# Performance work log

Measured on AMD Instinct MI355X. Metric: run time of the kernel, lower is better.

## Reference

```python
import jax, jax.numpy as jnp
import numpy as np

N_NODES = 32768
N_EDGES = 65536
NODE_IN = 4
EDGE_IN = 4
HIDDEN = 64
LN_EPS = 1e-5


def setup_inputs() -> dict:
    key = jax.random.key(0)
    ks = jax.random.split(key, 20)
    s = 0.05
    inp = {
        "x": jax.random.normal(ks[0], (N_NODES, NODE_IN), dtype=jnp.float32),
        "edge_attr": jax.random.normal(ks[1], (N_EDGES, EDGE_IN), dtype=jnp.float32),
        "edge_index": jax.random.randint(ks[2], (2, N_EDGES), 0, N_NODES, dtype=jnp.int64),
        "batch": jnp.zeros((N_NODES,), dtype=jnp.int64),
        # layer 1: edge MLP edge_in->64->node_in*hidden, root [node_in,hidden]
        "e1_w1": jax.random.normal(ks[3], (EDGE_IN, 64), dtype=jnp.float32) * s,
        "e1_b1": jnp.zeros((64,), jnp.float32),
        "e1_w2": jax.random.normal(ks[4], (64, NODE_IN * HIDDEN), dtype=jnp.float32) * s,
        "e1_b2": jnp.zeros((NODE_IN * HIDDEN,), jnp.float32),
        "root1": jax.random.normal(ks[5], (NODE_IN, HIDDEN), dtype=jnp.float32) * s,
        "bias1": jnp.zeros((HIDDEN,), jnp.float32),
        "ln1_g": jnp.ones((HIDDEN,), jnp.float32),
        "ln1_b": jnp.zeros((HIDDEN,), jnp.float32),
        # layer 2: edge MLP edge_in->128->hidden*hidden, root [hidden,hidden]
        "e2_w1": jax.random.normal(ks[6], (EDGE_IN, 128), dtype=jnp.float32) * s,
        "e2_b1": jnp.zeros((128,), jnp.float32),
        "e2_w2": jax.random.normal(ks[7], (128, HIDDEN * HIDDEN), dtype=jnp.float32) * s,
        "e2_b2": jnp.zeros((HIDDEN * HIDDEN,), jnp.float32),
        "root2": jax.random.normal(ks[8], (HIDDEN, HIDDEN), dtype=jnp.float32) * s,
        "bias2": jnp.zeros((HIDDEN,), jnp.float32),
        "ln2_g": jnp.ones((HIDDEN,), jnp.float32),
        "ln2_b": jnp.zeros((HIDDEN,), jnp.float32),
    }
    return inp


def _nnconv(x, src, dst, edge_attr, ew1, eb1, ew2, eb2, root, bias, n_nodes):
    # edge-conditioned weights: [E, in_ch, out_ch]
    in_ch = x.shape[1]
    out_ch = root.shape[1]
    h = jax.nn.relu(edge_attr @ ew1 + eb1) @ ew2 + eb2
    W = h.reshape(-1, in_ch, out_ch)
    # gather source features, per-edge matvec, scatter-mean to dest
    msg = jnp.einsum('ei,eio->eo', x[src], W)  # [E, out_ch]
    summed = jax.ops.segment_sum(msg, dst, num_segments=n_nodes)
    cnt = jax.ops.segment_sum(jnp.ones((dst.shape[0],), msg.dtype), dst,
                              num_segments=n_nodes)
    agg = summed / jnp.maximum(cnt, 1.0)[:, None]
    return agg + x @ root + bias


def _layernorm(x, g, b):
    m = x.mean(-1, keepdims=True)
    v = ((x - m) ** 2).mean(-1, keepdims=True)
    return (x - m) * jax.lax.rsqrt(v + LN_EPS) * g + b


def reference(x, edge_attr, e1_w1, e1_b1, e1_w2, e1_b2, root1, bias1, ln1_g, ln1_b,
              e2_w1, e2_b1, e2_w2, e2_b2, root2, bias2, ln2_g, ln2_b,
              edge_index, batch):
    src, dst = edge_index[0], edge_index[1]
    n = x.shape[0]
    h = _nnconv(x, src, dst, edge_attr, e1_w1, e1_b1, e1_w2, e1_b2, root1, bias1, n)
    h = _layernorm(jax.nn.relu(h), ln1_g, ln1_b)  # dropout = identity (eval)
    h = _nnconv(h, src, dst, edge_attr, e2_w1, e2_b1, e2_w2, e2_b2, root2, bias2, n)
    h = _layernorm(jax.nn.relu(h), ln2_g, ln2_b)
    # global mean pool (single graph -> [1, hidden])
    gs = jax.ops.segment_sum(h, batch, num_segments=1)
    gc = jax.ops.segment_sum(jnp.ones((n,), h.dtype), batch, num_segments=1)
    return gs / jnp.maximum(gc, 1.0)[:, None]
```

## Files before the change

### kernel.cpp

```cpp
#include <hip/hip_runtime.h>

#define N_NODES 32768
#define N_EDGES 65536

typedef float f32x4 __attribute__((ext_vector_type(4)));
typedef short s16x8 __attribute__((ext_vector_type(8)));

__device__ __forceinline__ unsigned short f2bf(float f){
  unsigned u = __float_as_uint(f);
  u += 0x7FFFu + ((u >> 16) & 1u);
  return (unsigned short)(u >> 16);
}
__device__ __forceinline__ float bf2f(unsigned short b){
  return __uint_as_float(((unsigned)b) << 16);
}

__global__ void k_zero(int* __restrict__ p, int n){
  int i = blockIdx.x * 256 + threadIdx.x;
  if (i < n) p[i] = 0;
}

__global__ void k_prep(const float* __restrict__ e2_w2, const float* __restrict__ e2_b2,
                       const float* __restrict__ e1_w2,
                       unsigned short* __restrict__ W2f, unsigned short* __restrict__ T1g){
  int idx = blockIdx.x * 256 + threadIdx.x;
  if (idx < 129 * 4096){
    int j = idx & 7, l = (idx >> 3) & 63, half = (idx >> 9) & 1, ot = (idx >> 10) & 3, kf = idx >> 12;
    int i = half * 32 + ((l >> 4) << 3) + j;
    int o = ot * 16 + (l & 15);
    float v = (kf < 128) ? e2_w2[kf * 4096 + i * 64 + o] : e2_b2[i * 64 + o];
    W2f[idx] = f2bf(v);
  } else if (idx < 129 * 4096 + 16384){
    int t = idx - 129 * 4096;
    int j = t & 7, l = (t >> 3) & 63, half = (t >> 9) & 1, ot = (t >> 10) & 3, i = t >> 12;
    int kf = half * 32 + ((l >> 4) << 3) + j;
    int o = ot * 16 + (l & 15);
    T1g[t] = f2bf(e1_w2[kf * 256 + i * 64 + o]);
  }
}

__global__ void k_hist(const int* __restrict__ ei, int* __restrict__ cnti){
  int i = blockIdx.x * 256 + threadIdx.x;
  if (i < N_EDGES) atomicAdd(cnti + ei[N_EDGES + i], 1);
}

__global__ void k_scanA(const int* __restrict__ cnti, int* __restrict__ lex, int* __restrict__ bsum){
  const int tid = threadIdx.x;
  int n = blockIdx.x * 256 + tid;
  int c = cnti[n];
  int v = c;
  int lane = tid & 63;
  #pragma unroll
  for (int d = 1; d < 64; d <<= 1){
    int t = __shfl_up(v, d);
    if (lane >= d) v += t;
  }
  __shared__ int wsum[4];
  if (lane == 63) wsum[tid >> 6] = v;
  __syncthreads();
  int off = 0;
  for (int i = 0; i < (tid >> 6); ++i) off += wsum[i];
  lex[n] = off + v - c;
  if (tid == 255) bsum[blockIdx.x] = off + v;
}

__global__ void k_scanB(const int* __restrict__ bsum, int* __restrict__ bsx){
  const int tid = threadIdx.x;
  int c = bsum[tid];
  int v = c;
  int lane = tid & 63;
  #pragma unroll
  for (int d = 1; d < 64; d <<= 1){
    int t = __shfl_up(v, d);
    if (lane >= d) v += t;
  }
  __shared__ int w0;
  if (tid == 63) w0 = v;
  __syncthreads();
  if (tid >= 64) v += w0;
  bsx[tid] = v - c;
}

__global__ void k_fill(const int* __restrict__ ei, const int* __restrict__ lex,
                       const int* __restrict__ bsx, int* __restrict__ cur,
                       int* __restrict__ eslot){
  int e = blockIdx.x * 256 + threadIdx.x;
  if (e < N_EDGES){
    int d = ei[N_EDGES + e];
    int base = lex[d] + bsx[d >> 8];
    eslot[e] = base + atomicAdd(cur + d, 1);
  }
}

__launch_bounds__(256, 4)
__global__ void k_msg1(const float* __restrict__ x, const float* __restrict__ ea,
                       const int* __restrict__ ei, const int* __restrict__ eslot,
                       const float* __restrict__ e1_w1, const float* __restrict__ e1_b1,
                       const float* __restrict__ e1_b2,
                       const unsigned short* __restrict__ T1g,
                       float* __restrict__ msg)
{
  __shared__ float eas[64 * 4];
  __shared__ unsigned short F1f[8 * 64 * 8];
  const int tid = threadIdx.x;
  const int eblk = blockIdx.x * 64;

  if (tid < 64) ((float4*)eas)[tid] = ((const float4*)ea)[eblk + tid];
  __syncthreads();
  {
    int kf = tid & 63, eh = tid >> 6;
    float w0 = e1_w1[kf], w1 = e1_w1[64 + kf], w2 = e1_w1[128 + kf], w3 = e1_w1[192 + kf];
    float bb = e1_b1[kf];
    int half = kf >> 5, hi = (kf >> 3) & 3, j = kf & 7;
    for (int e = eh * 16; e < eh * 16 + 16; ++e){
      float s = fmaf(eas[e*4+0], w0, fmaf(eas[e*4+1], w1, fmaf(eas[e*4+2], w2, fmaf(eas[e*4+3], w3, bb))));
      F1f[(((e >> 4) * 2 + half) * 64 + hi * 16 + (e & 15)) * 8 + j] = f2bf(fmaxf(s, 0.f));
    }
  }
  __syncthreads();

  const int l = tid & 63, lm = l & 15, lg = l >> 4;
  const int ot = tid >> 6;
  int esl[4];
  float xs[4][4];
  s16x8 bf[4][2];
  #pragma unroll
  for (int et = 0; et < 4; ++et){
    int e = eblk + et * 16 + lm;
    int s = ei[e];
    esl[et] = eslot[e];
    float4 xv = *(const float4*)(x + s * 4);
    xs[et][0] = xv.x; xs[et][1] = xv.y; xs[et][2] = xv.z; xs[et][3] = xv.w;
    bf[et][0] = ((const s16x8*)F1f)[(et * 2 + 0) * 64 + l];
    bf[et][1] = ((const s16x8*)F1f)[(et * 2 + 1) * 64 + l];
  }
  f32x4 acc[4];
  #pragma unroll
  for (int et = 0; et < 4; ++et) acc[et] = (f32x4){0.f, 0.f, 0.f, 0.f};

  #pragma unroll
  for (int i = 0; i < 4; ++i){
    const s16x8* p = (const s16x8*)(T1g + (i * 4 + ot) * 1024);
    s16x8 a0 = p[l], a1 = p[64 + l];
    #pragma unroll
    for (int et = 0; et < 4; ++et){
      f32x4 g = (f32x4){0.f, 0.f, 0.f, 0.f};
      g = __builtin_amdgcn_mfma_f32_16x16x32_bf16(a0, bf[et][0], g, 0, 0, 0);
      g = __builtin_amdgcn_mfma_f32_16x16x32_bf16(a1, bf[et][1], g, 0, 0, 0);
      acc[et] += xs[et][i] * g;
    }
  }
  float b2v[4][4];
  #pragma unroll
  for (int i = 0; i < 4; ++i)
    #pragma unroll
    for (int r = 0; r < 4; ++r) b2v[i][r] = e1_b2[i * 64 + ot * 16 + lg * 4 + r];
  #pragma unroll
  for (int et = 0; et < 4; ++et)
    #pragma unroll
    for (int r = 0; r < 4; ++r)
      #pragma unroll
      for (int i = 0; i < 4; ++i) acc[et][r] = fmaf(xs[et][i], b2v[i][r], acc[et][r]);

  #pragma unroll
  for (int et = 0; et < 4; ++et)
    *(f32x4*)(msg + (size_t)esl[et] * 64 + ot * 16 + lg * 4) = acc[et];
}

__launch_bounds__(256)
__global__ void k_node1(const float* __restrict__ x, const float* __restrict__ root1,
                        const float* __restrict__ bias1, const float* __restrict__ lng,
                        const float* __restrict__ lnb, const int* __restrict__ cnti,
                        const int* __restrict__ lex, const int* __restrict__ bsx,
                        const float* __restrict__ msg, unsigned short* __restrict__ h1b)
{
  const int tid = threadIdx.x;
  int n = blockIdx.x * 4 + (tid >> 6);
  int o = tid & 63;
  int rp = lex[n] + bsx[n >> 8];
  int deg = cnti[n];
  float s = 0.f;
  for (int j = 0; j < deg; ++j) s += msg[(size_t)(rp + j) * 64 + o];
  float v = s * (1.f / fmaxf((float)deg, 1.f));
  float4 xv = *(const float4*)(x + n * 4);
  v = fmaf(xv.x, root1[o], v);
  v = fmaf(xv.y, root1[64 + o], v);
  v = fmaf(xv.z, root1[128 + o], v);
  v = fmaf(xv.w, root1[192 + o], v);
  v = fmaxf(v + bias1[o], 0.f);
  float m = v;
  #pragma unroll
  for (int d = 32; d > 0; d >>= 1) m += __shfl_xor(m, d);
  m *= (1.f / 64.f);
  float dd = v - m;
  float var = dd * dd;
  #pragma unroll
  for (int d = 32; d > 0; d >>= 1) var += __shfl_xor(var, d);
  var *= (1.f / 64.f);
  float out = dd * rsqrtf(var + 1e-5f) * lng[o] + lnb[o];
  h1b[n * 64 + o] = f2bf(out);
}

__launch_bounds__(512, 4)
__global__ void k_msg2(const float* __restrict__ ea, const int* __restrict__ ei,
                       const int* __restrict__ eslot,
                       const float* __restrict__ e2_w1, const float* __restrict__ e2_b1,
                       const unsigned short* __restrict__ h1b,
                       const unsigned short* __restrict__ W2f,
                       float* __restrict__ msg)
{
  __shared__ float eas[128 * 4];
  __shared__ float F2s[128 * 132];
  const int tid = threadIdx.x;
  const int eblk = blockIdx.x * 128;
  if (tid < 128) ((float4*)eas)[tid] = ((const float4*)ea)[eblk + tid];
  __syncthreads();
  {
    int kf = tid & 127, q = tid >> 7;
    float w0 = e2_w1[kf], w1 = e2_w1[128 + kf], w2 = e2_w1[256 + kf], w3 = e2_w1[384 + kf];
    float bb = e2_b1[kf];
    for (int e = q * 32; e < q * 32 + 32; ++e){
      float s = fmaf(eas[e*4+0], w0, fmaf(eas[e*4+1], w1, fmaf(eas[e*4+2], w2, fmaf(eas[e*4+3], w3, bb))));
      F2s[e * 132 + kf] = fmaxf(s, 0.f);
    }
  }
  __syncthreads();

  const int w = tid >> 6, l = tid & 63, lm = l & 15, lg = l >> 4;
  const int ot = w >> 1, eh = w & 1;
  int f2base[4], esl[4];
  s16x8 bh[4][2];
  #pragma unroll
  for (int et = 0; et < 4; ++et){
    int eloc = eh * 64 + et * 16 + lm;
    int e = eblk + eloc;
    int s = ei[e];
    esl[et] = eslot[e];
    f2base[et] = eloc * 132;
    const s16x8* hp = (const s16x8*)(h1b + s * 64);
    bh[et][0] = hp[lg];
    bh[et][1] = hp[4 + lg];
  }
  f32x4 acc[4];
  #pragma unroll
  for (int et = 0; et < 4; ++et) acc[et] = (f32x4){0.f, 0.f, 0.f, 0.f};

  const unsigned short* wbase = W2f + ot * 1024;
  s16x8 A0[2], A1[2], A2[2], A3[2];
  #define LOADA(DST, KF) { const s16x8* p = (const s16x8*)(wbase + (size_t)(KF) * 4096); DST[0] = p[l]; DST[1] = p[64 + l]; }
  #define STEP(A, J) { \
    _Pragma("unroll") \
    for (int et = 0; et < 4; ++et){ \
      float f2v = f2c[et][J]; \
      f32x4 g = (f32x4){0.f, 0.f, 0.f, 0.f}; \
      g = __builtin_amdgcn_mfma_f32_16x16x32_bf16(A[0], bh[et][0], g, 0, 0, 0); \
      g = __builtin_amdgcn_mfma_f32_16x16x32_bf16(A[1], bh[et][1], g, 0, 0, 0); \
      acc[et] += f2v * g; \
    } }

  LOADA(A0, 0)
  LOADA(A1, 1)
  #pragma unroll 1
  for (int ch = 0; ch < 32; ++ch){
    f32x4 f2c[4];
    #pragma unroll
    for (int et = 0; et < 4; ++et) f2c[et] = *(const f32x4*)&F2s[f2base[et] + ch * 4];
    const int kf = ch * 4;
    LOADA(A2, kf + 2)
    STEP(A0, 0)
    LOADA(A3, kf + 3)
    STEP(A1, 1)
    LOADA(A0, kf + 4)
    STEP(A2, 2)
    const int k5 = (kf + 5 > 128) ? 128 : kf + 5;
    LOADA(A1, k5)
    STEP(A3, 3)
  }
  #pragma unroll
  for (int et = 0; et < 4; ++et){
    acc[et] = __builtin_amdgcn_mfma_f32_16x16x32_bf16(A0[0], bh[et][0], acc[et], 0, 0, 0);
    acc[et] = __builtin_amdgcn_mfma_f32_16x16x32_bf16(A0[1], bh[et][1], acc[et], 0, 0, 0);
  }
  #undef LOADA
  #undef STEP

  #pragma unroll
  for (int et = 0; et < 4; ++et)
    *(f32x4*)(msg + (size_t)esl[et] * 64 + ot * 16 + lg * 4) = acc[et];
}

__launch_bounds__(1024)
__global__ void k_node2(const unsigned short* __restrict__ h1b, const float* __restrict__ root2,
                        const float* __restrict__ bias2, const float* __restrict__ lng,
                        const float* __restrict__ lnb, const int* __restrict__ cnti,
                        const int* __restrict__ lex, const int* __restrict__ bsx,
                        const float* __restrict__ msg, float* __restrict__ partial)
{
  const int tid = threadIdx.x;
  int n = blockIdx.x * 16 + (tid >> 6);
  int o = tid & 63;
  int rp = lex[n] + bsx[n >> 8];
  int deg = cnti[n];
  float s = 0.f;
  for (int j = 0; j < deg; ++j) s += msg[(size_t)(rp + j) * 64 + o];
  float v = s * (1.f / fmaxf((float)deg, 1.f));
  const s16x8* hp = (const s16x8*)(h1b + n * 64);
  #pragma unroll
  for (int c = 0; c < 8; ++c){
    s16x8 hv = hp[c];
    #pragma unroll
    for (int j = 0; j < 8; ++j)
      v = fmaf(bf2f((unsigned short)hv[j]), root2[(c * 8 + j) * 64 + o], v);
  }
  v = fmaxf(v + bias2[o], 0.f);
  float m = v;
  #pragma unroll
  for (int d = 32; d > 0; d >>= 1) m += __shfl_xor(m, d);
  m *= (1.f / 64.f);
  float dd = v - m;
  float var = dd * dd;
  #pragma unroll
  for (int d = 32; d > 0; d >>= 1) var += __shfl_xor(var, d);
  var *= (1.f / 64.f);
  float out = dd * rsqrtf(var + 1e-5f) * lng[o] + lnb[o];
  __shared__ float pp[16][64];
  pp[tid >> 6][o] = out;
  __syncthreads();
  if (tid < 64){
    float t = 0.f;
    #pragma unroll
    for (int k = 0; k < 16; ++k) t += pp[k][tid];
    partial[blockIdx.x * 64 + tid] = t;
  }
}

__launch_bounds__(1024)
__global__ void k_out(const float* __restrict__ partial, float* __restrict__ out){
  const int tid = threadIdx.x;
  int o = tid & 63, q = tid >> 6;
  float s = 0.f;
  for (int b = q; b < 2048; b += 16) s += partial[b * 64 + o];
  __shared__ float pp[16][64];
  pp[q][o] = s;
  __syncthreads();
  if (tid < 64){
    float t = 0.f;
    #pragma unroll
    for (int k = 0; k < 16; ++k) t += pp[k][tid];
    out[tid] = t * (1.f / 32768.f);
  }
}

extern "C" void kernel_launch(void* const* d_in, const int* in_sizes, int n_in,
                              void* d_out, int out_size, void* d_ws, size_t ws_size,
                              hipStream_t stream)
{
  const float* x      = (const float*)d_in[0];
  const float* ea     = (const float*)d_in[1];
  const int*   ei     = (const int*)  d_in[2];
  const float* e1_w1  = (const float*)d_in[4];
  const float* e1_b1  = (const float*)d_in[5];
  const float* e1_w2  = (const float*)d_in[6];
  const float* e1_b2  = (const float*)d_in[7];
  const float* root1  = (const float*)d_in[8];
  const float* bias1  = (const float*)d_in[9];
  const float* ln1g   = (const float*)d_in[10];
  const float* ln1b   = (const float*)d_in[11];
  const float* e2_w1  = (const float*)d_in[12];
  const float* e2_b1  = (const float*)d_in[13];
  const float* e2_w2  = (const float*)d_in[14];
  const float* e2_b2  = (const float*)d_in[15];
  const float* root2  = (const float*)d_in[16];
  const float* bias2  = (const float*)d_in[17];
  const float* ln2g   = (const float*)d_in[18];
  const float* ln2b   = (const float*)d_in[19];

  char* w = (char*)d_ws;
  float*          msg     = (float*)(w);
  unsigned short* h1b     = (unsigned short*)(w + 16777216);
  unsigned short* W2f     = (unsigned short*)(w + 20971520);
  unsigned short* T1g     = (unsigned short*)(w + 22028288);
  int*            cnti    = (int*)(w + 22061056);
  int*            cur     = (int*)(w + 22192128);
  int*            lex     = (int*)(w + 22323200);
  int*            bsx     = (int*)(w + 22454272);
  int*            bsum    = (int*)(w + 22454784);
  int*            eslot   = (int*)(w + 22455296);
  float*          partial = (float*)(w + 22717440);

  k_zero <<<256, 256, 0, stream>>>(cnti, 65536);
  k_prep <<<2128, 256, 0, stream>>>(e2_w2, e2_b2, e1_w2, W2f, T1g);
  k_hist <<<256, 256, 0, stream>>>(ei, cnti);
  k_scanA<<<128, 256, 0, stream>>>(cnti, lex, bsum);
  k_scanB<<<1, 128, 0, stream>>>(bsum, bsx);
  k_fill <<<256, 256, 0, stream>>>(ei, lex, bsx, cur, eslot);
  k_msg1 <<<1024, 256, 0, stream>>>(x, ea, ei, eslot, e1_w1, e1_b1, e1_b2, T1g, msg);
  k_node1<<<8192, 256, 0, stream>>>(x, root1, bias1, ln1g, ln1b, cnti, lex, bsx, msg, h1b);
  k_msg2 <<<512, 512, 0, stream>>>(ea, ei, eslot, e2_w1, e2_b1, h1b, W2f, msg);
  k_node2<<<2048, 1024, 0, stream>>>(h1b, root2, bias2, ln2g, ln2b, cnti, lex, bsx, msg, partial);
  k_out  <<<1, 1024, 0, stream>>>(partial, (float*)d_out);
}
```

Before: 175.9 us.

## Halve k_msg2 block size so each wave covers all 128 edges with grouped weight prefetch

k_msg2 now runs 256 threads (4 waves) per block instead of 512, and each wave handles one 16-wide output tile across all 128 edges (8 edge tiles) rather than 64 edges. This doubles reuse of each loaded W2f fragment and halves global weight traffic per block. Weight loads are also grouped four k-steps at a time and double-buffered (GA/GB), and the source-feature gathers are moved ahead of the F2 computation to overlap latency. The cost is much higher register pressure (8 accumulators, 8x2 B fragments, 2x4x2 A buffers), and occupancy is lower with launch bounds of (256,2).

```diff
diff --git a/kernel.cpp b/kernel.cpp
--- a/kernel.cpp
+++ b/kernel.cpp
@@ -201,7 +201,7 @@
   h1b[n * 64 + o] = f2bf(out);
 }
 
-__launch_bounds__(512, 4)
+__launch_bounds__(256, 2)
 __global__ void k_msg2(const float* __restrict__ ea, const int* __restrict__ ei,
                        const int* __restrict__ eslot,
                        const float* __restrict__ e2_w1, const float* __restrict__ e2_b1,
@@ -213,79 +213,79 @@
   __shared__ float F2s[128 * 132];
   const int tid = threadIdx.x;
   const int eblk = blockIdx.x * 128;
+  const int l = tid & 63, lm = l & 15, lg = l >> 4;
+  const int ot = tid >> 6;
+
+  int esl[8];
+  s16x8 bh[8][2];
+  #pragma unroll
+  for (int et = 0; et < 8; ++et){
+    int e = eblk + et * 16 + lm;
+    int s = ei[e];
+    esl[et] = eslot[e];
+    const s16x8* hp = (const s16x8*)(h1b + s * 64);
+    bh[et][0] = hp[lg];
+    bh[et][1] = hp[4 + lg];
+  }
+
   if (tid < 128) ((float4*)eas)[tid] = ((const float4*)ea)[eblk + tid];
   __syncthreads();
   {
     int kf = tid & 127, q = tid >> 7;
     float w0 = e2_w1[kf], w1 = e2_w1[128 + kf], w2 = e2_w1[256 + kf], w3 = e2_w1[384 + kf];
     float bb = e2_b1[kf];
-    for (int e = q * 32; e < q * 32 + 32; ++e){
+    for (int e = q * 64; e < q * 64 + 64; ++e){
       float s = fmaf(eas[e*4+0], w0, fmaf(eas[e*4+1], w1, fmaf(eas[e*4+2], w2, fmaf(eas[e*4+3], w3, bb))));
       F2s[e * 132 + kf] = fmaxf(s, 0.f);
     }
   }
   __syncthreads();
 
-  const int w = tid >> 6, l = tid & 63, lm = l & 15, lg = l >> 4;
-  const int ot = w >> 1, eh = w & 1;
-  int f2base[4], esl[4];
-  s16x8 bh[4][2];
-  #pragma unroll
-  for (int et = 0; et < 4; ++et){
-    int eloc = eh * 64 + et * 16 + lm;
-    int e = eblk + eloc;
-    int s = ei[e];
-    esl[et] = eslot[e];
-    f2base[et] = eloc * 132;
-    const s16x8* hp = (const s16x8*)(h1b + s * 64);
-    bh[et][0] = hp[lg];
-    bh[et][1] = hp[4 + lg];
-  }
-  f32x4 acc[4];
-  #pragma unroll
-  for (int et = 0; et < 4; ++et) acc[et] = (f32x4){0.f, 0.f, 0.f, 0.f};
+  f32x4 acc[8];
+  #pragma unroll
+  for (int et = 0; et < 8; ++et) acc[et] = (f32x4){0.f, 0.f, 0.f, 0.f};
 
   const unsigned short* wbase = W2f + ot * 1024;
-  s16x8 A0[2], A1[2], A2[2], A3[2];
-  #define LOADA(DST, KF) { const s16x8* p = (const s16x8*)(wbase + (size_t)(KF) * 4096); DST[0] = p[l]; DST[1] = p[64 + l]; }
-  #define STEP(A, J) { \
+  s16x8 GA[4][2], GB[4][2];
+  #define LDG(BUF, G) { \
     _Pragma("unroll") \
-    for (int et = 0; et < 4; ++et){ \
-      float f2v = f2c[et][J]; \
-      f32x4 g = (f32x4){0.f, 0.f, 0.f, 0.f}; \
-      g = __builtin_amdgcn_mfma_f32_16x16x32_bf16(A[0], bh[et][0], g, 0, 0, 0); \
-      g = __builtin_amdgcn_mfma_f32_16x16x32_bf16(A[1], bh[et][1], g, 0, 0, 0); \
-      acc[et] += f2v * g; \
+    for (int s = 0; s < 4; ++s){ \
+      int kf = (G) * 4 + s; if (kf > 128) kf = 128; \
+      const s16x8* p = (const s16x8*)(wbase + (size_t)kf * 4096); \
+      BUF[s][0] = p[l]; BUF[s][1] = p[64 + l]; \
     } }
-
-  LOADA(A0, 0)
-  LOADA(A1, 1)
+  #define CMP(BUF, G) { \
+    f32x4 f2c[8]; \
+    _Pragma("unroll") \
+    for (int et = 0; et < 8; ++et) f2c[et] = *(const f32x4*)&F2s[(et * 16 + lm) * 132 + (G) * 4]; \
+    _Pragma("unroll") \
+    for (int s = 0; s < 4; ++s){ \
+      _Pragma("unroll") \
+      for (int et = 0; et < 8; ++et){ \
+        f32x4 g = (f32x4){0.f, 0.f, 0.f, 0.f}; \
+        g = __builtin_amdgcn_mfma_f32_16x16x32_bf16(BUF[s][0], bh[et][0], g, 0, 0, 0); \
+        g = __builtin_amdgcn_mfma_f32_16x16x32_bf16(BUF[s][1], bh[et][1], g, 0, 0, 0); \
+        acc[et] += f2c[et][s] * g; \
+      } } }
+
+  LDG(GA, 0)
   #pragma unroll 1
-  for (int ch = 0; ch < 32; ++ch){
-    f32x4 f2c[4];
-    #pragma unroll
-    for (int et = 0; et < 4; ++et) f2c[et] = *(const f32x4*)&F2s[f2base[et] + ch * 4];
-    const int kf = ch * 4;
-    LOADA(A2, kf + 2)
-    STEP(A0, 0)
-    LOADA(A3, kf + 3)
-    STEP(A1, 1)
-    LOADA(A0, kf + 4)
-    STEP(A2, 2)
-    const int k5 = (kf + 5 > 128) ? 128 : kf + 5;
-    LOADA(A1, k5)
-    STEP(A3, 3)
-  }
-  #pragma unroll
-  for (int et = 0; et < 4; ++et){
-    acc[et] = __builtin_amdgcn_mfma_f32_16x16x32_bf16(A0[0], bh[et][0], acc[et], 0, 0, 0);
-    acc[et] = __builtin_amdgcn_mfma_f32_16x16x32_bf16(A0[1], bh[et][1], acc[et], 0, 0, 0);
-  }
-  #undef LOADA
-  #undef STEP
-
-  #pragma unroll
-  for (int et = 0; et < 4; ++et)
+  for (int g2 = 0; g2 < 32; g2 += 2){
+    LDG(GB, g2 + 1)
+    CMP(GA, g2)
+    LDG(GA, g2 + 2)
+    CMP(GB, g2 + 1)
+  }
+  #pragma unroll
+  for (int et = 0; et < 8; ++et){
+    acc[et] = __builtin_amdgcn_mfma_f32_16x16x32_bf16(GA[0][0], bh[et][0], acc[et], 0, 0, 0);
+    acc[et] = __builtin_amdgcn_mfma_f32_16x16x32_bf16(GA[0][1], bh[et][1], acc[et], 0, 0, 0);
+  }
+  #undef LDG
+  #undef CMP
+
+  #pragma unroll
+  for (int et = 0; et < 8; ++et)
     *(f32x4*)(msg + (size_t)esl[et] * 64 + ot * 16 + lg * 4) = acc[et];
 }
 
@@ -396,7 +396,7 @@
   k_fill <<<256, 256, 0, stream>>>(ei, lex, bsx, cur, eslot);
   k_msg1 <<<1024, 256, 0, stream>>>(x, ea, ei, eslot, e1_w1, e1_b1, e1_b2, T1g, msg);
   k_node1<<<8192, 256, 0, stream>>>(x, root1, bias1, ln1g, ln1b, cnti, lex, bsx, msg, h1b);
-  k_msg2 <<<512, 512, 0, stream>>>(ea, ei, eslot, e2_w1, e2_b1, h1b, W2f, msg);
+  k_msg2 <<<512, 256, 0, stream>>>(ea, ei, eslot, e2_w1, e2_b1, h1b, W2f, msg);
   k_node2<<<2048, 1024, 0, stream>>>(h1b, root2, bias2, ln2g, ln2b, cnti, lex, bsx, msg, partial);
   k_out  <<<1, 1024, 0, stream>>>(partial, (float*)d_out);
 }
```

Result: no change. 177.9 us (+1.1%).
